# Optimization experiments

Hardware: AMD Instinct MI355X
Metric: run time of the kernel (lower is better)

## Reference

```python
import jax, jax.numpy as jnp
import numpy as np

# Production-scale dims: CSA layer on a 64x64, 512-channel decoder feature map
B, C, H, W = 8, 512, 64, 64
HOLE = 32  # centered square hole side -> M = 1024 masked points, N = 3072 context points
EPS = 1e-8


def _mask_and_indices():
    m = np.zeros((H, W), np.float32)
    r0, c0 = (H - HOLE) // 2, (W - HOLE) // 2
    m[r0:r0 + HOLE, c0:c0 + HOLE] = 1.0
    flat = m.reshape(-1)
    mask_idx = np.nonzero(flat > 0.5)[0].astype(np.int32)      # masked (hole) flat positions, raster order
    nonmask_idx = np.nonzero(flat <= 0.5)[0].astype(np.int32)  # known (context) flat positions
    return m, nonmask_idx, mask_idx


def setup_inputs() -> dict:
    key = jax.random.key(0)
    x = jax.random.normal(key, (B, C, H, W), dtype=jnp.float32)
    m, nm, mi = _mask_and_indices()
    return {
        "input": x,
        "mask": jnp.asarray(m),
        "nonmask_point_idx": jnp.asarray(nm),
        "mask_point_idx": jnp.asarray(mi),
    }


def _csa(x, nonmask_point_idx, mask_point_idx):
    """Coherent Semantic Attention with 1x1 patches (shift_sz=1, stride=1).

    For each masked location (raster order): find the most-similar context
    patch by cosine similarity, then coherently blend it with the previously
    generated patch, weighted by their respective similarities.
    """
    b, c, h, w = x.shape
    feats = x.reshape(b, c, h * w)                      # [B,C,HW] 1x1 patches
    ctx = feats[:, :, nonmask_point_idx]                # [B,C,N] known/context patches
    msk = feats[:, :, mask_point_idx]                   # [B,C,M] masked patches
    ctx_n = ctx / (jnp.linalg.norm(ctx, axis=1, keepdims=True) + EPS)
    msk_n = msk / (jnp.linalg.norm(msk, axis=1, keepdims=True) + EPS)

    # cross cosine similarity: dominant compute (B*M*N*C)
    cos = jnp.einsum('bcm,bcn->bmn', msk_n, ctx_n)      # [B,M,N]
    maxc = cos.max(axis=-1)                             # [B,M] best context similarity
    amax = cos.argmax(axis=-1)                          # [B,M]
    # gather the best-matching (unnormalized) context patch per masked point
    best = jnp.take_along_axis(ctx.transpose(0, 2, 1), amax[..., None], axis=1)  # [B,M,C]

    xs = (msk_n.transpose(2, 0, 1),   # [M,B,C] normalized masked patches
          best.transpose(1, 0, 2),    # [M,B,C] best context patches
          maxc.T)                     # [M,B]

    def step(prev, inp):
        mn, bst, mx = inp
        prev_n = prev / (jnp.linalg.norm(prev, axis=-1, keepdims=True) + EPS)
        d_ad = jnp.maximum(jnp.sum(mn * prev_n, axis=-1), 0.0)   # [B] coherence with previous generated patch
        cur = (d_ad[:, None] * prev + mx[:, None] * bst) / (d_ad + mx + EPS)[:, None]
        return cur, cur

    # prev initialized to zeros -> d_ad = 0 for the first masked patch (pure context copy)
    _, gen = jax.lax.scan(step, jnp.zeros((b, c), x.dtype), xs)   # [M,B,C]

    out = feats.at[:, :, mask_point_idx].set(gen.transpose(1, 2, 0))
    return out.reshape(b, c, h, w)


def reference(input, mask, nonmask_point_idx, mask_point_idx):
    return _csa(input, nonmask_point_idx, mask_point_idx)
```

## Files before the change

kernel.cpp:

```cpp
#include <hip/hip_runtime.h>
#include <hip/hip_bf16.h>

#define B_   8
#define C_   512
#define HW_  4096
#define M_   1024
#define N_   3072
#define EPS_ 1e-8f

typedef __attribute__((ext_vector_type(4))) float f32x4;
typedef __attribute__((ext_vector_type(8))) short short8;

__global__ void k_norms(const float* __restrict__ x, float* __restrict__ inv_all) {
    int blk = blockIdx.x;
    int b = blk >> 5;
    int chunk = blk & 31;
    int hw = chunk * 128 + threadIdx.x;
    const float* xb = x + (size_t)b * C_ * HW_;
    float acc = 0.f;
#pragma unroll 8
    for (int c = 0; c < C_; ++c) {
        float v = xb[(size_t)c * HW_ + hw];
        acc = fmaf(v, v, acc);
    }
    inv_all[b * HW_ + hw] = 1.0f / (sqrtf(acc) + EPS_);
}

__global__ __launch_bounds__(256) void k_pack(const float* __restrict__ x,
    const int* __restrict__ nm_idx, const int* __restrict__ m_idx,
    const float* __restrict__ inv_all,
    unsigned int* __restrict__ Apk, unsigned int* __restrict__ Bpk,
    float* __restrict__ invM, float* __restrict__ invC)
{
    __shared__ float T[32][513];
    __shared__ int ps[32];
    int blk = blockIdx.x;
    int t = threadIdx.x;
    int isA = blk < 256;
    int b, grp;
    const int* idxarr;
    if (isA) { b = blk >> 5; grp = blk & 31; idxarr = m_idx; }
    else     { int r = blk - 256; b = r / 96; grp = r % 96; idxarr = nm_idx; }
    const float* xb = x + (size_t)b * C_ * HW_;
    if (t < 32) {
        int p = idxarr[grp * 32 + t];
        ps[t] = p;
        float iv = inv_all[b * HW_ + p];
        if (isA) invM[b * 1024 + grp * 32 + t] = iv;
        else     invC[b * 3072 + grp * 32 + t] = iv;
    }
    __syncthreads();
#pragma unroll 4
    for (int rep = 0; rep < 64; ++rep) {
        int idx = rep * 256 + t;
        int c = idx >> 5, i = idx & 31;
        T[i][c] = xb[(size_t)c * HW_ + ps[i]];
    }
    __syncthreads();
    unsigned int* dst = isA ? (Apk + ((size_t)b * 1024 + grp * 32) * 512)
                            : (Bpk + ((size_t)b * 3072 + grp * 32) * 512);
#pragma unroll 4
    for (int rep = 0; rep < 64; ++rep) {
        int idx = rep * 256 + t;
        int i = idx >> 9, c = idx & 511;
        float v = T[i][c];
        __hip_bfloat16 h = __float2bfloat16(v);
        float hf = __bfloat162float(h);
        __hip_bfloat16 l = __float2bfloat16(v - hf);
        unsigned int hi = __bfloat16_as_ushort(h);
        unsigned int lo = __bfloat16_as_ushort(l);
        dst[(size_t)i * 512 + c] = (lo << 16) | hi;
    }
}

__global__ __launch_bounds__(256, 2) void k_cosm(
    const unsigned int* __restrict__ Apk, const unsigned int* __restrict__ Bpk,
    const float* __restrict__ invM, const float* __restrict__ invC,
    float* __restrict__ pmax, int* __restrict__ pidx)
{
    __shared__ unsigned int As[128 * 36];
    __shared__ unsigned int Bs[128 * 36];
    __shared__ float sInvM[128];
    __shared__ float sInvC[128];

    int blk = blockIdx.x;
    int b  = blk / 192;
    int r  = blk % 192;
    int mt = r / 24;
    int nt = r % 24;
    int m0 = mt * 128, n0 = nt * 128;
    int t = threadIdx.x;
    int w = t >> 6, lane = t & 63;
    int wm = (w & 1) * 64, wn = (w >> 1) * 64;
    int quad = lane >> 4, nl = lane & 15;

    if (t < 128) sInvM[t] = invM[b * 1024 + m0 + t];
    else         sInvC[t - 128] = invC[b * 3072 + n0 + (t - 128)];

    const unsigned int* gA = Apk + ((size_t)b * 1024 + m0) * 512;
    const unsigned int* gB = Bpk + ((size_t)b * 3072 + n0) * 512;

    f32x4 acc[4][4];
#pragma unroll
    for (int i = 0; i < 4; ++i)
#pragma unroll
        for (int j = 0; j < 4; ++j) acc[i][j] = (f32x4){0.f, 0.f, 0.f, 0.f};

    for (int kt = 0; kt < 16; ++kt) {
        int k0 = kt * 32;
        __syncthreads();
#pragma unroll
        for (int rep = 0; rep < 4; ++rep) {
            int idx = rep * 1024 + t * 4;
            int row = idx >> 5, col = idx & 31;
            uint4 va = *(const uint4*)(gA + (size_t)row * 512 + k0 + col);
            uint4 vb = *(const uint4*)(gB + (size_t)row * 512 + k0 + col);
            *(uint4*)&As[row * 36 + col] = va;
            *(uint4*)&Bs[row * 36 + col] = vb;
        }
        __syncthreads();

        short8 ah[4], al[4], bh[4], bl[4];
#pragma unroll
        for (int mt2 = 0; mt2 < 4; ++mt2) {
            int m = wm + mt2 * 16 + nl;
            uint4 q0 = *(const uint4*)&As[m * 36 + quad * 8];
            uint4 q1 = *(const uint4*)&As[m * 36 + quad * 8 + 4];
            uint4 H, L;
            H.x = __builtin_amdgcn_perm(q0.y, q0.x, 0x05040100u);
            H.y = __builtin_amdgcn_perm(q0.w, q0.z, 0x05040100u);
            H.z = __builtin_amdgcn_perm(q1.y, q1.x, 0x05040100u);
            H.w = __builtin_amdgcn_perm(q1.w, q1.z, 0x05040100u);
            L.x = __builtin_amdgcn_perm(q0.y, q0.x, 0x07060302u);
            L.y = __builtin_amdgcn_perm(q0.w, q0.z, 0x07060302u);
            L.z = __builtin_amdgcn_perm(q1.y, q1.x, 0x07060302u);
            L.w = __builtin_amdgcn_perm(q1.w, q1.z, 0x07060302u);
            ah[mt2] = *(short8*)&H; al[mt2] = *(short8*)&L;
        }
#pragma unroll
        for (int nt2 = 0; nt2 < 4; ++nt2) {
            int n = wn + nt2 * 16 + nl;
            uint4 q0 = *(const uint4*)&Bs[n * 36 + quad * 8];
            uint4 q1 = *(const uint4*)&Bs[n * 36 + quad * 8 + 4];
            uint4 H, L;
            H.x = __builtin_amdgcn_perm(q0.y, q0.x, 0x05040100u);
            H.y = __builtin_amdgcn_perm(q0.w, q0.z, 0x05040100u);
            H.z = __builtin_amdgcn_perm(q1.y, q1.x, 0x05040100u);
            H.w = __builtin_amdgcn_perm(q1.w, q1.z, 0x05040100u);
            L.x = __builtin_amdgcn_perm(q0.y, q0.x, 0x07060302u);
            L.y = __builtin_amdgcn_perm(q0.w, q0.z, 0x07060302u);
            L.z = __builtin_amdgcn_perm(q1.y, q1.x, 0x07060302u);
            L.w = __builtin_amdgcn_perm(q1.w, q1.z, 0x07060302u);
            bh[nt2] = *(short8*)&H; bl[nt2] = *(short8*)&L;
        }
#pragma unroll
        for (int mt2 = 0; mt2 < 4; ++mt2)
#pragma unroll
            for (int nt2 = 0; nt2 < 4; ++nt2) {
                acc[mt2][nt2] = __builtin_amdgcn_mfma_f32_16x16x32_bf16(
                    ah[mt2], bh[nt2], acc[mt2][nt2], 0, 0, 0);
                acc[mt2][nt2] = __builtin_amdgcn_mfma_f32_16x16x32_bf16(
                    ah[mt2], bl[nt2], acc[mt2][nt2], 0, 0, 0);
                acc[mt2][nt2] = __builtin_amdgcn_mfma_f32_16x16x32_bf16(
                    al[mt2], bh[nt2], acc[mt2][nt2], 0, 0, 0);
            }
    }

#pragma unroll
    for (int mt2 = 0; mt2 < 4; ++mt2)
#pragma unroll
        for (int reg = 0; reg < 4; ++reg) {
            int ml = wm + mt2 * 16 + quad * 4 + reg;
            float im = sInvM[ml];
            float v1 = -3.402823466e38f, v2 = -3.402823466e38f;
            int i1 = 0x7fffffff, i2 = 0x7fffffff;
#pragma unroll
            for (int nt2 = 0; nt2 < 4; ++nt2) {
                int nlc = wn + nt2 * 16 + nl;
                float v = acc[mt2][nt2][reg] * im * sInvC[nlc];
                int n = n0 + nlc;
                if (v > v1 || (v == v1 && n < i1)) { v2 = v1; i2 = i1; v1 = v; i1 = n; }
                else if (v > v2 || (v == v2 && n < i2)) { v2 = v; i2 = n; }
            }
#pragma unroll
            for (int off = 1; off < 16; off <<= 1) {
                float o1v = __shfl_xor(v1, off, 64); int o1i = __shfl_xor(i1, off, 64);
                float o2v = __shfl_xor(v2, off, 64); int o2i = __shfl_xor(i2, off, 64);
                if (o1v > v1 || (o1v == v1 && o1i < i1)) { v2 = v1; i2 = i1; v1 = o1v; i1 = o1i; }
                else if (o1v > v2 || (o1v == v2 && o1i < i2)) { v2 = o1v; i2 = o1i; }
                if (o2v > v1 || (o2v == v1 && o2i < i1)) { v2 = v1; i2 = i1; v1 = o2v; i1 = o2i; }
                else if (o2v > v2 || (o2v == v2 && o2i < i2)) { v2 = o2v; i2 = o2i; }
            }
            if (nl == 0) {
                int m_glob = (b << 10) + m0 + ml;
                int slot = nt * 2 + (w >> 1);
                int o = (m_glob * 48 + slot) * 2;
                pmax[o + 0] = v1; pidx[o + 0] = i1;
                pmax[o + 1] = v2; pidx[o + 1] = i2;
            }
        }
}

__global__ void k_combine(const float* __restrict__ x,
    const int* __restrict__ nm_idx, const int* __restrict__ m_idx,
    const float* __restrict__ pmax, const int* __restrict__ pidx,
    float* __restrict__ maxc, int* __restrict__ bestp)
{
    int id = blockIdx.x * 256 + threadIdx.x;
    int b = id >> 10, m = id & 1023;
    float v1 = -3.402823466e38f, v2 = -3.402823466e38f;
    int i1 = 0x7fffffff, i2 = 0x7fffffff;
#pragma unroll 8
    for (int r = 0; r < 96; ++r) {
        float v = pmax[(size_t)id * 96 + r];
        int   n = pidx[(size_t)id * 96 + r];
        if (v > v1 || (v == v1 && n < i1)) { v2 = v1; i2 = i1; v1 = v; i1 = n; }
        else if (v > v2 || (v == v2 && n < i2)) { v2 = v; i2 = n; }
    }
    if (v1 - v2 < 1e-4f) {
        const float* xb = x + (size_t)b * C_ * HW_;
        int pm = m_idx[m], p1 = nm_idx[i1], p2 = nm_idx[i2];
        double smm = 0, s11 = 0, s22 = 0, sm1 = 0, sm2 = 0;
        for (int c = 0; c < C_; ++c) {
            double xm = xb[(size_t)c * HW_ + pm];
            double xa = xb[(size_t)c * HW_ + p1];
            double xc = xb[(size_t)c * HW_ + p2];
            smm += xm * xm; s11 += xa * xa; s22 += xc * xc;
            sm1 += xm * xa; sm2 += xm * xc;
        }
        double inv_m = 1.0 / (sqrt(smm) + 1e-8);
        double c1 = sm1 * inv_m / (sqrt(s11) + 1e-8);
        double c2 = sm2 * inv_m / (sqrt(s22) + 1e-8);
        if (c2 > c1 || (c2 == c1 && i2 < i1)) { v1 = v2; i1 = i2; }
    }
    maxc[id]  = v1;
    bestp[id] = nm_idx[i1];
}

__global__ void k_copy(const float4* __restrict__ in, float4* __restrict__ out) {
    int idx = blockIdx.x * 256 + threadIdx.x;
    int stride = gridDim.x * 256;
    for (int i = idx; i < (B_ * C_ * HW_ / 4); i += stride) out[i] = in[i];
}

__global__ __launch_bounds__(256) void k_gather(const float* __restrict__ x,
    const int* __restrict__ m_idx, const float* __restrict__ inv_all,
    const int* __restrict__ bestp, float* __restrict__ mskn, float* __restrict__ best)
{
    __shared__ float T[32][513];
    __shared__ int ps[32]; __shared__ float invm[32]; __shared__ int bp[32];
    int blk = blockIdx.x;
    int b = blk >> 5, row = blk & 31;
    int m0 = row * 32;
    int t = threadIdx.x;
    const float* xb = x + (size_t)b * C_ * HW_;
    if (t < 32) {
        int p = m_idx[m0 + t];
        ps[t] = p; invm[t] = inv_all[b * HW_ + p];
        bp[t] = bestp[(b << 10) + m0 + t];
    }
    __syncthreads();
#pragma unroll 4
    for (int rep = 0; rep < 64; ++rep) {
        int idx = rep * 256 + t;
        int c = idx >> 5, i = idx & 31;
        T[i][c] = xb[(size_t)c * HW_ + ps[i]];
    }
    __syncthreads();
#pragma unroll 4
    for (int rep = 0; rep < 64; ++rep) {
        int idx = rep * 256 + t;
        int i = idx >> 9, c = idx & 511;
        mskn[((size_t)(b << 10) + m0 + i) * C_ + c] = T[i][c] * invm[i];
    }
    for (int mi = 0; mi < 32; ++mi) {
        int p = bp[mi];
        size_t o = ((size_t)(b << 10) + m0 + mi) * C_;
        for (int c = t; c < C_; c += 256)
            best[o + c] = xb[(size_t)c * HW_ + p];
    }
}

__device__ __forceinline__ float wave_sum64(float x) {
    x += __int_as_float(__builtin_amdgcn_update_dpp(0, __float_as_int(x), 0x111, 0xf, 0xf, false));
    x += __int_as_float(__builtin_amdgcn_update_dpp(0, __float_as_int(x), 0x112, 0xf, 0xf, false));
    x += __int_as_float(__builtin_amdgcn_update_dpp(0, __float_as_int(x), 0x114, 0xf, 0xf, false));
    x += __int_as_float(__builtin_amdgcn_update_dpp(0, __float_as_int(x), 0x118, 0xf, 0xf, false));
    x += __int_as_float(__builtin_amdgcn_update_dpp(0, __float_as_int(x), 0x142, 0xa, 0xf, false));
    x += __int_as_float(__builtin_amdgcn_update_dpp(0, __float_as_int(x), 0x143, 0xc, 0xf, false));
    return __int_as_float(__builtin_amdgcn_readlane(__float_as_int(x), 63));
}

__global__ __launch_bounds__(64, 1) void k_scan(const float* __restrict__ mskn,
    const float* __restrict__ best, const float* __restrict__ maxc,
    float* __restrict__ gen)
{
    int b = blockIdx.x;
    int lane = threadIdx.x;
    const float4* mn4 = (const float4*)(mskn + (size_t)b * M_ * C_);
    const float4* bs4 = (const float4*)(best + (size_t)b * M_ * C_);
    const float* mx_p = maxc + b * M_;
    float4* gen4 = (float4*)(gen + (size_t)b * M_ * C_);

    float pr[8];
#pragma unroll
    for (int j = 0; j < 8; ++j) pr[j] = 0.f;

    float4 mf[8][2], bf[8][2]; float mx[8];
#pragma unroll
    for (int s = 0; s < 7; ++s) {
        int base = s * 128 + lane * 2;
        mf[s][0] = mn4[base]; mf[s][1] = mn4[base + 1];
        bf[s][0] = bs4[base]; bf[s][1] = bs4[base + 1];
        mx[s] = mx_p[s];
    }

    for (int mb = 0; mb < 128; ++mb) {
#pragma unroll
        for (int mi = 0; mi < 8; ++mi) {
            int m = mb * 8 + mi;
            int cur = mi;
            int nxt = (mi + 7) & 7;
            if (m + 7 < M_) {
                int base = (m + 7) * 128 + lane * 2;
                mf[nxt][0] = mn4[base]; mf[nxt][1] = mn4[base + 1];
                bf[nxt][0] = bs4[base]; bf[nxt][1] = bs4[base + 1];
                mx[nxt] = mx_p[m + 7];
            }
            float mn[8] = {mf[cur][0].x, mf[cur][0].y, mf[cur][0].z, mf[cur][0].w,
                           mf[cur][1].x, mf[cur][1].y, mf[cur][1].z, mf[cur][1].w};
            float bs[8] = {bf[cur][0].x, bf[cur][0].y, bf[cur][0].z, bf[cur][0].w,
                           bf[cur][1].x, bf[cur][1].y, bf[cur][1].z, bf[cur][1].w};
            float s1a = 0.f, s1b = 0.f, s2a = 0.f, s2b = 0.f;
#pragma unroll
            for (int j = 0; j < 4; ++j) {
                s1a = fmaf(pr[j], pr[j], s1a);
                s1b = fmaf(pr[j + 4], pr[j + 4], s1b);
                s2a = fmaf(mn[j], pr[j], s2a);
                s2b = fmaf(mn[j + 4], pr[j + 4], s2b);
            }
            float s1 = wave_sum64(s1a + s1b);
            float s2 = wave_sum64(s2a + s2b);
            float mxc = mx[cur];
            float d_ad = fmaxf(s2, 0.f) * __builtin_amdgcn_rcpf(sqrtf(s1) + EPS_);
            float inv  = __builtin_amdgcn_rcpf(d_ad + mxc + EPS_);
#pragma unroll
            for (int j = 0; j < 8; ++j)
                pr[j] = (d_ad * pr[j] + mxc * bs[j]) * inv;
            float4 o0 = {pr[0], pr[1], pr[2], pr[3]};
            float4 o1 = {pr[4], pr[5], pr[6], pr[7]};
            gen4[m * 128 + lane * 2]     = o0;
            gen4[m * 128 + lane * 2 + 1] = o1;
        }
    }
}

__global__ __launch_bounds__(256) void k_scatter(const float* __restrict__ gen,
    const int* __restrict__ m_idx, float* __restrict__ out)
{
    __shared__ float T[32][513];
    int blk = blockIdx.x;
    int b = blk >> 5, row = blk & 31;
    int m0 = row * 32;
    int t = threadIdx.x;
#pragma unroll 4
    for (int rep = 0; rep < 64; ++rep) {
        int idx = rep * 256 + t;
        int i = idx >> 9, c = idx & 511;
        T[i][c] = gen[((size_t)(b << 10) + m0 + i) * C_ + c];
    }
    __syncthreads();
    int colg = m_idx[m0];
    float* outb = out + (size_t)b * C_ * HW_;
#pragma unroll 4
    for (int rep = 0; rep < 64; ++rep) {
        int idx = rep * 256 + t;
        int c = idx >> 5, i = idx & 31;
        outb[(size_t)c * HW_ + colg + i] = T[i][c];
    }
}

extern "C" void kernel_launch(void* const* d_in, const int* in_sizes, int n_in,
                              void* d_out, int out_size, void* d_ws, size_t ws_size,
                              hipStream_t stream) {
    (void)in_sizes; (void)n_in; (void)out_size; (void)ws_size;
    const float* x      = (const float*)d_in[0];
    const int*   nm_idx = (const int*)d_in[2];
    const int*   m_idx  = (const int*)d_in[3];
    float* out = (float*)d_out;
    char* ws = (char*)d_ws;

    float* inv_all = (float*)(ws + 0);
    float* invM    = (float*)(ws + 131072);
    float* invC    = (float*)(ws + 163840);
    float* pmax    = (float*)(ws + 262144);
    int*   pidx    = (int*)  (ws + 3407872);
    float* maxc    = (float*)(ws + 6553600);
    int*   bestp   = (int*)  (ws + 6586368);
    unsigned int* Apk = (unsigned int*)(ws + 6619136);
    unsigned int* Bpk = (unsigned int*)(ws + 23396352);
    float* mskn = (float*)Apk;
    float* best = (float*)Bpk;
    float* gen  = (float*)(ws + 23396352 + 16777216);

    hipLaunchKernelGGL(k_norms,   dim3(256),  dim3(128), 0, stream, x, inv_all);
    hipLaunchKernelGGL(k_pack,    dim3(1024), dim3(256), 0, stream, x, nm_idx, m_idx, inv_all, Apk, Bpk, invM, invC);
    hipLaunchKernelGGL(k_cosm,    dim3(1536), dim3(256), 0, stream, Apk, Bpk, invM, invC, pmax, pidx);
    hipLaunchKernelGGL(k_combine, dim3(32),   dim3(256), 0, stream, x, nm_idx, m_idx, pmax, pidx, maxc, bestp);
    hipLaunchKernelGGL(k_copy,    dim3(2048), dim3(256), 0, stream, (const float4*)x, (float4*)out);
    hipLaunchKernelGGL(k_gather,  dim3(256),  dim3(256), 0, stream, x, m_idx, inv_all, bestp, mskn, best);
    hipLaunchKernelGGL(k_scan,    dim3(8),    dim3(64),  0, stream, mskn, best, maxc, gen);
    hipLaunchKernelGGL(k_scatter, dim3(256),  dim3(256), 0, stream, gen, m_idx, out);
}
```

Baseline: 733.0 us.

## Stage scan inputs through an async global-to-LDS ring buffer

The sequential scan kernel used to prefetch upcoming masked and best-context rows into a register ring. It now issues global_load_lds copies six steps ahead into an eight-slot LDS ring, with explicit vmcnt waits and inline ds_read_b128 loads. The maxc values are also preloaded into shared memory once. The aim is to hide global-load latency on this latency-bound, one-wave-per-batch recurrence while freeing registers. In exchange it depends on hand-tuned waitcnt counts that also count the stores, which makes it fragile.

```diff
diff --git a/kernel.cpp b/kernel.cpp
--- a/kernel.cpp
+++ b/kernel.cpp
@@ -291,67 +291,97 @@
     return __int_as_float(__builtin_amdgcn_readlane(__float_as_int(x), 63));
 }
 
+__device__ __forceinline__ void stage_slot(const float* gm, const float* gb,
+                                           float* slot ) {
+    typedef const __attribute__((address_space(1))) unsigned int GU;
+    typedef __attribute__((address_space(3))) unsigned int LU;
+    __builtin_amdgcn_global_load_lds((GU*)(gm),       (LU*)(slot),       16, 0, 0);
+    __builtin_amdgcn_global_load_lds((GU*)(gm + 256), (LU*)(slot + 256), 16, 0, 0);
+    __builtin_amdgcn_global_load_lds((GU*)(gb),       (LU*)(slot + 512), 16, 0, 0);
+    __builtin_amdgcn_global_load_lds((GU*)(gb + 256), (LU*)(slot + 768), 16, 0, 0);
+}
+
+#define WAIT_VMCNT(N) asm volatile("s_waitcnt vmcnt(" #N ")" ::: "memory")
+
+#define SCAN_STEP(mexpr, NLIT) do {                                          \
+    int m_ = (mexpr);                                                        \
+    if (m_ + 6 < M_)                                                         \
+        stage_slot(mskn_b + (size_t)(m_ + 6) * 512 + lane * 4,               \
+                   best_b + (size_t)(m_ + 6) * 512 + lane * 4,               \
+                   &ring[((m_ + 6) & 7) << 10]);                             \
+    WAIT_VMCNT(NLIT);                                                        \
+    __builtin_amdgcn_sched_barrier(0);                                       \
+    unsigned lb_ = ringBase + ((unsigned)(m_ & 7) << 12) + lane * 32u;       \
+    f32x4 r0, r1, r2, r3;                                                    \
+    asm volatile("ds_read_b128 %0, %4 offset:0\n\t"                          \
+                 "ds_read_b128 %1, %4 offset:16\n\t"                         \
+                 "ds_read_b128 %2, %4 offset:2048\n\t"                       \
+                 "ds_read_b128 %3, %4 offset:2064\n\t"                       \
+                 "s_waitcnt lgkmcnt(0)"                                      \
+                 : "=&v"(r0), "=&v"(r1), "=&v"(r2), "=&v"(r3)                \
+                 : "v"(lb_));                                                \
+    __builtin_amdgcn_sched_barrier(0);                                       \
+    float mn[8] = {r0.x, r0.y, r0.z, r0.w, r1.x, r1.y, r1.z, r1.w};          \
+    float bs[8] = {r2.x, r2.y, r2.z, r2.w, r3.x, r3.y, r3.z, r3.w};          \
+    float s1a = 0.f, s1b = 0.f, s2a = 0.f, s2b = 0.f;                        \
+    _Pragma("unroll")                                                        \
+    for (int j = 0; j < 4; ++j) {                                            \
+        s1a = fmaf(pr[j], pr[j], s1a);                                       \
+        s1b = fmaf(pr[j + 4], pr[j + 4], s1b);                               \
+        s2a = fmaf(mn[j], pr[j], s2a);                                       \
+        s2b = fmaf(mn[j + 4], pr[j + 4], s2b);                               \
+    }                                                                        \
+    float s1 = wave_sum64(s1a + s1b);                                        \
+    float s2 = wave_sum64(s2a + s2b);                                        \
+    float mxc = smx[m_];                                                     \
+    float d_ad = fmaxf(s2, 0.f) * __builtin_amdgcn_rcpf(sqrtf(s1) + EPS_);   \
+    float inv  = __builtin_amdgcn_rcpf(d_ad + mxc + EPS_);                   \
+    _Pragma("unroll")                                                        \
+    for (int j = 0; j < 8; ++j)                                              \
+        pr[j] = (d_ad * pr[j] + mxc * bs[j]) * inv;                          \
+    float4 o0 = {pr[0], pr[1], pr[2], pr[3]};                                \
+    float4 o1 = {pr[4], pr[5], pr[6], pr[7]};                                \
+    gen4[m_ * 128 + lane * 2]     = o0;                                      \
+    gen4[m_ * 128 + lane * 2 + 1] = o1;                                      \
+} while (0)
+
 __global__ __launch_bounds__(64, 1) void k_scan(const float* __restrict__ mskn,
     const float* __restrict__ best, const float* __restrict__ maxc,
     float* __restrict__ gen)
 {
+    __shared__ float ring[8 * 1024];
+    __shared__ float smx[M_];
     int b = blockIdx.x;
     int lane = threadIdx.x;
-    const float4* mn4 = (const float4*)(mskn + (size_t)b * M_ * C_);
-    const float4* bs4 = (const float4*)(best + (size_t)b * M_ * C_);
+    const float* mskn_b = mskn + (size_t)b * M_ * C_;
+    const float* best_b = best + (size_t)b * M_ * C_;
     const float* mx_p = maxc + b * M_;
     float4* gen4 = (float4*)(gen + (size_t)b * M_ * C_);
 
+    unsigned ringBase = (unsigned)(size_t)(__attribute__((address_space(3))) float*)&ring[0];
+
+#pragma unroll
+    for (int i = 0; i < 16; ++i) smx[i * 64 + lane] = mx_p[i * 64 + lane];
+
     float pr[8];
 #pragma unroll
     for (int j = 0; j < 8; ++j) pr[j] = 0.f;
 
-    float4 mf[8][2], bf[8][2]; float mx[8];
-#pragma unroll
-    for (int s = 0; s < 7; ++s) {
-        int base = s * 128 + lane * 2;
-        mf[s][0] = mn4[base]; mf[s][1] = mn4[base + 1];
-        bf[s][0] = bs4[base]; bf[s][1] = bs4[base + 1];
-        mx[s] = mx_p[s];
-    }
-
-    for (int mb = 0; mb < 128; ++mb) {
+#pragma unroll
+    for (int s = 0; s < 6; ++s)
+        stage_slot(mskn_b + (size_t)s * 512 + lane * 4,
+                   best_b + (size_t)s * 512 + lane * 4,
+                   &ring[(s & 7) << 10]);
+
+    for (int mb = 0; mb < 127; ++mb) {
 #pragma unroll
         for (int mi = 0; mi < 8; ++mi) {
-            int m = mb * 8 + mi;
-            int cur = mi;
-            int nxt = (mi + 7) & 7;
-            if (m + 7 < M_) {
-                int base = (m + 7) * 128 + lane * 2;
-                mf[nxt][0] = mn4[base]; mf[nxt][1] = mn4[base + 1];
-                bf[nxt][0] = bs4[base]; bf[nxt][1] = bs4[base + 1];
-                mx[nxt] = mx_p[m + 7];
-            }
-            float mn[8] = {mf[cur][0].x, mf[cur][0].y, mf[cur][0].z, mf[cur][0].w,
-                           mf[cur][1].x, mf[cur][1].y, mf[cur][1].z, mf[cur][1].w};
-            float bs[8] = {bf[cur][0].x, bf[cur][0].y, bf[cur][0].z, bf[cur][0].w,
-                           bf[cur][1].x, bf[cur][1].y, bf[cur][1].z, bf[cur][1].w};
-            float s1a = 0.f, s1b = 0.f, s2a = 0.f, s2b = 0.f;
-#pragma unroll
-            for (int j = 0; j < 4; ++j) {
-                s1a = fmaf(pr[j], pr[j], s1a);
-                s1b = fmaf(pr[j + 4], pr[j + 4], s1b);
-                s2a = fmaf(mn[j], pr[j], s2a);
-                s2b = fmaf(mn[j + 4], pr[j + 4], s2b);
-            }
-            float s1 = wave_sum64(s1a + s1b);
-            float s2 = wave_sum64(s2a + s2b);
-            float mxc = mx[cur];
-            float d_ad = fmaxf(s2, 0.f) * __builtin_amdgcn_rcpf(sqrtf(s1) + EPS_);
-            float inv  = __builtin_amdgcn_rcpf(d_ad + mxc + EPS_);
-#pragma unroll
-            for (int j = 0; j < 8; ++j)
-                pr[j] = (d_ad * pr[j] + mxc * bs[j]) * inv;
-            float4 o0 = {pr[0], pr[1], pr[2], pr[3]};
-            float4 o1 = {pr[4], pr[5], pr[6], pr[7]};
-            gen4[m * 128 + lane * 2]     = o0;
-            gen4[m * 128 + lane * 2 + 1] = o1;
-        }
+            SCAN_STEP(mb * 8 + mi, 24);
+        }
+    }
+#pragma unroll
+    for (int mi = 0; mi < 8; ++mi) {
+        SCAN_STEP(1016 + mi, 0);
     }
 }
 
```

Measured after the change: 736.2 us. Within noise of the previous version (+0.4%).
